# Optimization experiments

Measured on AMD Instinct MI355X. Metric: run time of the kernel, lower is better.

The kernel has to match this reference:

```python
import jax, jax.numpy as jnp
from jax import lax
import numpy as np

B, C, H, W, T = 8, 256, 31, 31, 7  # batch, channels, search HxW, template size


def setup_inputs() -> dict:
    key = jax.random.key(0)
    k1, k2, k3, k4 = jax.random.split(key, 4)
    sr = jax.random.normal(k1, (B, C, H, W), jnp.float32)
    tmpl = jax.random.normal(k2, (B, C, T, T), jnp.float32)
    # offset/mask conv params (module zero-inits; use small random as a trained stand-in)
    w_om = jax.random.normal(k3, (3 * T * T, C, 3, 3), jnp.float32) * 0.01
    b_om = jax.random.normal(k4, (3 * T * T,), jnp.float32) * 0.01
    return {"sr_features": sr, "template_features": tmpl,
            "w_offset_mask": w_om, "b_offset_mask": b_om}


def _modulated_deform_xcorr(sr, tmpl, w_om, b_om):
    Bs, Cs, Hs, Ws = sr.shape
    Ts = tmpl.shape[-1]
    K = Ts * Ts
    # 3x3 'same' conv predicting per-pixel offsets (y, x) and modulation mask
    om = lax.conv_general_dilated(sr, w_om, (1, 1), 'SAME',
                                  dimension_numbers=('NCHW', 'OIHW', 'NCHW'))
    om = om + b_om[None, :, None, None]
    off_y, off_x, mask = om[:, :K], om[:, K:2 * K], om[:, 2 * K:]
    mask = jax.nn.sigmoid(mask)
    oh, ow = Hs - Ts + 1, Ws - Ts + 1  # stride 1, padding 0, dilation 1
    off_y = off_y[:, :, :oh, :ow]
    off_x = off_x[:, :, :oh, :ow]
    mask = mask[:, :, :oh, :ow]
    # kernel-tap base offsets (k = p*T + q)
    ky = jnp.repeat(jnp.arange(Ts), Ts).astype(sr.dtype)  # (K,)
    kx = jnp.tile(jnp.arange(Ts), Ts).astype(sr.dtype)    # (K,)
    iy = jnp.arange(oh, dtype=sr.dtype)
    ix = jnp.arange(ow, dtype=sr.dtype)
    ys = iy[None, None, :, None] + ky[None, :, None, None] + off_y  # (B,K,oh,ow)
    xs = ix[None, None, None, :] + kx[None, :, None, None] + off_x  # (B,K,oh,ow)
    y0 = jnp.floor(ys)
    x0 = jnp.floor(xs)
    wy = ys - y0
    wx = xs - x0
    bidx = jnp.arange(Bs)[:, None, None, None]

    def gather(yf, xf):
        # zero-padded gather at integer corner (yf, xf); returns (B,K,oh,ow,C)
        valid = (yf >= 0) & (yf <= Hs - 1) & (xf >= 0) & (xf <= Ws - 1)
        yc = jnp.clip(yf, 0, Hs - 1).astype(jnp.int32)
        xc = jnp.clip(xf, 0, Ws - 1).astype(jnp.int32)
        v = sr[bidx, :, yc, xc]  # (B,K,oh,ow,C)
        return v * valid[..., None].astype(sr.dtype)

    one = jnp.asarray(1, sr.dtype)
    v = (((one - wy) * (one - wx))[..., None] * gather(y0, x0)
         + ((one - wy) * wx)[..., None] * gather(y0, x0 + 1)
         + (wy * (one - wx))[..., None] * gather(y0 + 1, x0)
         + (wy * wx)[..., None] * gather(y0 + 1, x0 + 1))
    # depthwise xcorr: template acts as per-(batch,channel) kernel, modulated by mask
    tmpl_k = tmpl.reshape(Bs, Cs, K)
    out = jnp.einsum('bck,bkij,bkijc->bcij', tmpl_k, mask, v)  # (B,C,oh,ow)
    return out


def reference(sr_features, template_features, w_offset_mask, b_offset_mask):
    return _modulated_deform_xcorr(sr_features, template_features,
                                   w_offset_mask, b_offset_mask)
```

## Files before the change

### kernel.cpp

```cpp
#include <hip/hip_runtime.h>
#include <hip/hip_bf16.h>
#include <math.h>

#define B_ 8
#define C_ 256
#define H_ 31
#define W_ 31
#define T_ 7
#define K_ 49
#define OC_ 147
#define OCP 160
#define OH_ 25
#define OW_ 25
#define NSP 961
#define OSP 625
#define KK_ 2304

typedef __bf16 bf16x8 __attribute__((ext_vector_type(8)));
typedef float f32x4 __attribute__((ext_vector_type(4)));

#define OFFB_SRT 0
#define OFFB_TMT 3936256
#define OFFB_WPK 4136960
#define OFFB_BIAS 4874240
#define OFFB_OM  4874880

__device__ inline float blo(unsigned u) { return __uint_as_float(u << 16); }
__device__ inline float bhi(unsigned u) { return __uint_as_float(u & 0xffff0000u); }

__global__ __launch_bounds__(256) void prep(const float* __restrict__ sr,
                                            const float* __restrict__ tm,
                                            const float* __restrict__ w,
                                            const float* __restrict__ bias,
                                            __hip_bfloat16* __restrict__ srT,
                                            __hip_bfloat16* __restrict__ tmT,
                                            __hip_bfloat16* __restrict__ wPk,
                                            float* __restrict__ biasP) {
    __shared__ float tile[32][33];
    int bid = blockIdx.x;
    int t = threadIdx.x;

    if (bid < 1984) {
        int b = bid / 248;
        int rem = bid % 248;
        int ct = rem / 31;
        int st = rem % 31;
        int c0 = ct * 32, s0 = st * 32;
        int tx = t & 31, ty = t >> 5;
        #pragma unroll
        for (int rr = 0; rr < 4; rr++) {
            int c = c0 + ty + rr * 8;
            int s = s0 + tx;
            if (s < NSP) tile[ty + rr * 8][tx] = sr[(b * C_ + c) * NSP + s];
        }
        __syncthreads();
        #pragma unroll
        for (int rr = 0; rr < 4; rr++) {
            int s = s0 + ty + rr * 8;
            int c = c0 + tx;
            if (s < NSP) srT[((long)b * NSP + s) * C_ + c] = __float2bfloat16(tile[tx][ty + rr * 8]);
        }
    } else if (bid < 2376) {
        int bx = bid - 1984;
        int b = bx / K_;
        int k = bx % K_;
        tmT[(b * K_ + k) * C_ + t] = __float2bfloat16(tm[(b * C_ + t) * K_ + k]);
    } else {
        if (bid == 2376 && t < OCP)
            biasP[t] = (t < OC_) ? bias[t] : 0.f;
        int i = (bid - 2376) * 256 + t;
        if (i < 46080) {
            int l = i & 63;
            int fid = i >> 6;
            int mf = fid % 5;
            int mh = (fid / 5) % 2;
            int ks = (fid / 10) % 2;
            int s  = (fid / 20) % 9;
            int cg = fid / 180;
            int oc = mh * 80 + mf * 16 + (l & 15);
            int cbase = cg * 64 + ks * 32 + (l >> 4) * 8;
            bf16x8 v;
            #pragma unroll
            for (int jj = 0; jj < 8; jj++) {
                float f = (oc < OC_) ? w[oc * KK_ + (cbase + jj) * 9 + s] : 0.f;
                v[jj] = (__bf16)f;
            }
            *reinterpret_cast<bf16x8*>(wPk + ((long)i << 3)) = v;
        }
    }
}

__global__ __launch_bounds__(128) void k3_mfma(const __hip_bfloat16* __restrict__ srT,
                                               const __hip_bfloat16* __restrict__ wPk,
                                               float* __restrict__ om) {
    __shared__ __hip_bfloat16 lds[88 * 72];
    int sb = (blockIdx.x & 7) * 100 + (blockIdx.x >> 3);
    int b = sb / 100;
    int rem = sb % 100;
    int i = rem / 4;
    int cg = rem % 4;
    int tid = threadIdx.x;

    const __hip_bfloat16* srTb = srT + (long)b * NSP * C_ + cg * 64;
    for (int o = tid; o < 648; o += 128) {
        int ryx = o >> 3;
        int c8 = (o & 7) * 8;
        int yy = ryx / 27;
        int xi = ryx - yy * 27;
        int y = i - 1 + yy;
        int x = xi - 1;
        bf16x8 v = {};
        if (y >= 0 && x >= 0)
            v = *reinterpret_cast<const bf16x8*>(srTb + (y * W_ + x) * C_ + c8);
        *reinterpret_cast<bf16x8*>(&lds[ryx * 72 + c8]) = v;
    }
    __syncthreads();

    int wv = tid >> 6;
    int l = tid & 63;
    int lr = l & 15, lg = l >> 4;

    f32x4 acc[5][2] = {};
    const bf16x8* apk = reinterpret_cast<const bf16x8*>(wPk);

    #pragma unroll
    for (int dy = 0; dy < 3; ++dy) {
        #pragma unroll
        for (int dx = 0; dx < 3; ++dx) {
            int s = dy * 3 + dx;
            #pragma unroll
            for (int ks = 0; ks < 2; ++ks) {
                int e0 = (dy * 27 + dx + lr) * 72 + ks * 32 + lg * 8;
                bf16x8 b0 = *reinterpret_cast<const bf16x8*>(&lds[e0]);
                bf16x8 b1 = *reinterpret_cast<const bf16x8*>(&lds[e0 + 16 * 72]);
                const bf16x8* ap = apk + (long)((((cg * 9 + s) * 2 + ks) * 2 + wv) * 5) * 64 + l;
                #pragma unroll
                for (int mf = 0; mf < 5; ++mf) {
                    bf16x8 a = ap[mf * 64];
                    acc[mf][0] = __builtin_amdgcn_mfma_f32_16x16x32_bf16(a, b0, acc[mf][0], 0, 0, 0);
                    acc[mf][1] = __builtin_amdgcn_mfma_f32_16x16x32_bf16(a, b1, acc[mf][1], 0, 0, 0);
                }
            }
        }
    }

    #pragma unroll
    for (int nf = 0; nf < 2; ++nf) {
        int j = nf * 16 + lr;
        if (j < OW_) {
            float* ob = om + (long)((b * OH_ + i) * 4 + cg) * (OW_ * OCP) + j * OCP + wv * 80 + lg * 4;
            #pragma unroll
            for (int mf = 0; mf < 5; ++mf)
                *reinterpret_cast<f32x4*>(ob + mf * 16) = acc[mf][nf];
        }
    }
}

__global__ __launch_bounds__(64) void k4_gather(const __hip_bfloat16* __restrict__ srT,
                                                const __hip_bfloat16* __restrict__ tmT,
                                                const float* __restrict__ om,
                                                const float* __restrict__ biasP,
                                                float* __restrict__ out) {
    __shared__ float lom[OCP];
    __shared__ int4 loff[K_];
    __shared__ float4 lwt[K_];
    int sb = (blockIdx.x & 7) * 625 + (blockIdx.x >> 3);
    int b = sb / OSP;
    int rem = sb % OSP;
    int i = rem / OW_;
    int j = rem % OW_;
    int t = threadIdx.x;

    if (t < 40) {
        f32x4 s = *reinterpret_cast<const f32x4*>(biasP + t * 4);
        const float* ob = om + (long)(b * OH_ + i) * (4 * OW_ * OCP) + j * OCP + t * 4;
        #pragma unroll
        for (int cg = 0; cg < 4; cg++)
            s += *reinterpret_cast<const f32x4*>(ob + cg * (OW_ * OCP));
        *reinterpret_cast<f32x4*>(lom + t * 4) = s;
    }
    __syncthreads();

    if (t < K_) {
        float oy = lom[t];
        float ox = lom[K_ + t];
        float mk = 1.f / (1.f + expf(-lom[2 * K_ + t]));
        float ys = (float)(i + t / T_) + oy;
        float xs = (float)(j + t % T_) + ox;
        float y0f = floorf(ys);
        float x0f = floorf(xs);
        float wy = ys - y0f, wx = xs - x0f;
        bool vy0 = (y0f >= 0.f) && (y0f <= 30.f);
        bool vy1 = (y0f >= -1.f) && (y0f <= 29.f);
        bool vx0 = (x0f >= 0.f) && (x0f <= 30.f);
        bool vx1 = (x0f >= -1.f) && (x0f <= 29.f);
        int iy = (int)y0f;
        int ix = (int)x0f;
        int cy0 = min(max(iy, 0), 30), cy1 = min(max(iy + 1, 0), 30);
        int cx0 = min(max(ix, 0), 30), cx1 = min(max(ix + 1, 0), 30);
        float a00 = (1.f - wy) * (1.f - wx), a01 = (1.f - wy) * wx;
        float a10 = wy * (1.f - wx), a11 = wy * wx;
        lwt[t] = make_float4(mk * a00 * (float)(vy0 && vx0),
                             mk * a01 * (float)(vy0 && vx1),
                             mk * a10 * (float)(vy1 && vx0),
                             mk * a11 * (float)(vy1 && vx1));
        loff[t] = make_int4((cy0 * W_ + cx0) * 64, (cy0 * W_ + cx1) * 64,
                            (cy1 * W_ + cx0) * 64, (cy1 * W_ + cx1) * 64);
    }
    __syncthreads();

    const uint2* srU = reinterpret_cast<const uint2*>(srT) + (long)b * NSP * 64;
    const uint2* tmU = reinterpret_cast<const uint2*>(tmT) + (long)b * K_ * 64;
    float a0 = 0.f, a1 = 0.f, a2 = 0.f, a3 = 0.f;

    for (int k = 0; k < K_; ++k) {
        int4 o = loff[k];
        float4 wt = lwt[k];
        uint2 u00 = srU[o.x + t];
        uint2 u01 = srU[o.y + t];
        uint2 u10 = srU[o.z + t];
        uint2 u11 = srU[o.w + t];
        uint2 tu  = tmU[(k << 6) + t];
        float s;
        s = wt.x * blo(u00.x); s = fmaf(wt.y, blo(u01.x), s);
        s = fmaf(wt.z, blo(u10.x), s); s = fmaf(wt.w, blo(u11.x), s);
        a0 = fmaf(blo(tu.x), s, a0);
        s = wt.x * bhi(u00.x); s = fmaf(wt.y, bhi(u01.x), s);
        s = fmaf(wt.z, bhi(u10.x), s); s = fmaf(wt.w, bhi(u11.x), s);
        a1 = fmaf(bhi(tu.x), s, a1);
        s = wt.x * blo(u00.y); s = fmaf(wt.y, blo(u01.y), s);
        s = fmaf(wt.z, blo(u10.y), s); s = fmaf(wt.w, blo(u11.y), s);
        a2 = fmaf(blo(tu.y), s, a2);
        s = wt.x * bhi(u00.y); s = fmaf(wt.y, bhi(u01.y), s);
        s = fmaf(wt.z, bhi(u10.y), s); s = fmaf(wt.w, bhi(u11.y), s);
        a3 = fmaf(bhi(tu.y), s, a3);
    }

    long ob = ((long)(b * C_ + 4 * t) * OH_ + i) * OW_ + j;
    out[ob] = a0;
    out[ob + OSP] = a1;
    out[ob + 2 * OSP] = a2;
    out[ob + 3 * OSP] = a3;
}

extern "C" void kernel_launch(void* const* d_in, const int* in_sizes, int n_in,
                              void* d_out, int out_size, void* d_ws, size_t ws_size,
                              hipStream_t stream) {
    const float* sr = (const float*)d_in[0];
    const float* tm = (const float*)d_in[1];
    const float* w  = (const float*)d_in[2];
    const float* bs = (const float*)d_in[3];
    float* out = (float*)d_out;
    char* wsb = (char*)d_ws;
    __hip_bfloat16* srT = (__hip_bfloat16*)(wsb + OFFB_SRT);
    __hip_bfloat16* tmT = (__hip_bfloat16*)(wsb + OFFB_TMT);
    __hip_bfloat16* wPk = (__hip_bfloat16*)(wsb + OFFB_WPK);
    float* biasP = (float*)(wsb + OFFB_BIAS);
    float* om = (float*)(wsb + OFFB_OM);

    prep<<<2556, 256, 0, stream>>>(sr, tm, w, bs, srT, tmT, wPk, biasP);
    k3_mfma<<<B_ * OH_ * 4, 128, 0, stream>>>(srT, wPk, om);
    k4_gather<<<B_ * OSP, 64, 0, stream>>>(srT, tmT, om, biasP, out);
}
```

Measured before the change: 139.6 us.

## Pack four pixels per block and split taps across half-waves with 16B loads

```diff
diff --git a/kernel.cpp b/kernel.cpp
--- a/kernel.cpp
+++ b/kernel.cpp
@@ -156,91 +156,118 @@
     }
 }
 
-__global__ __launch_bounds__(64) void k4_gather(const __hip_bfloat16* __restrict__ srT,
-                                                const __hip_bfloat16* __restrict__ tmT,
-                                                const float* __restrict__ om,
-                                                const float* __restrict__ biasP,
-                                                float* __restrict__ out) {
-    __shared__ float lom[OCP];
-    __shared__ int4 loff[K_];
-    __shared__ float4 lwt[K_];
-    int sb = (blockIdx.x & 7) * 625 + (blockIdx.x >> 3);
-    int b = sb / OSP;
-    int rem = sb % OSP;
-    int i = rem / OW_;
-    int j = rem % OW_;
-    int t = threadIdx.x;
-
-    if (t < 40) {
-        f32x4 s = *reinterpret_cast<const f32x4*>(biasP + t * 4);
-        const float* ob = om + (long)(b * OH_ + i) * (4 * OW_ * OCP) + j * OCP + t * 4;
+__global__ __launch_bounds__(256) void k4_gather(const __hip_bfloat16* __restrict__ srT,
+                                                 const __hip_bfloat16* __restrict__ tmT,
+                                                 const float* __restrict__ om,
+                                                 const float* __restrict__ biasP,
+                                                 float* __restrict__ out) {
+    __shared__ float lom[4][OCP];
+    __shared__ int4 loff[4][52];
+    __shared__ float4 lwt[4][52];
+    int wvp = threadIdx.x >> 6;
+    int l = threadIdx.x & 63;
+    int blk = (blockIdx.x & 7) * 157 + (blockIdx.x >> 3);
+    int pix = blk * 4 + wvp;
+    bool active = pix < B_ * OSP;
+    int b = 0, i = 0, j = 0;
+    if (active) {
+        b = pix / OSP;
+        int rem = pix % OSP;
+        i = rem / OW_;
+        j = rem % OW_;
+    }
+
+    if (active && l < 40) {
+        f32x4 s = *reinterpret_cast<const f32x4*>(biasP + l * 4);
+        const float* ob = om + (long)(b * OH_ + i) * (4 * OW_ * OCP) + j * OCP + l * 4;
         #pragma unroll
         for (int cg = 0; cg < 4; cg++)
             s += *reinterpret_cast<const f32x4*>(ob + cg * (OW_ * OCP));
-        *reinterpret_cast<f32x4*>(lom + t * 4) = s;
+        *reinterpret_cast<f32x4*>(&lom[wvp][l * 4]) = s;
     }
     __syncthreads();
 
-    if (t < K_) {
-        float oy = lom[t];
-        float ox = lom[K_ + t];
-        float mk = 1.f / (1.f + expf(-lom[2 * K_ + t]));
-        float ys = (float)(i + t / T_) + oy;
-        float xs = (float)(j + t % T_) + ox;
-        float y0f = floorf(ys);
-        float x0f = floorf(xs);
-        float wy = ys - y0f, wx = xs - x0f;
-        bool vy0 = (y0f >= 0.f) && (y0f <= 30.f);
-        bool vy1 = (y0f >= -1.f) && (y0f <= 29.f);
-        bool vx0 = (x0f >= 0.f) && (x0f <= 30.f);
-        bool vx1 = (x0f >= -1.f) && (x0f <= 29.f);
-        int iy = (int)y0f;
-        int ix = (int)x0f;
-        int cy0 = min(max(iy, 0), 30), cy1 = min(max(iy + 1, 0), 30);
-        int cx0 = min(max(ix, 0), 30), cx1 = min(max(ix + 1, 0), 30);
-        float a00 = (1.f - wy) * (1.f - wx), a01 = (1.f - wy) * wx;
-        float a10 = wy * (1.f - wx), a11 = wy * wx;
-        lwt[t] = make_float4(mk * a00 * (float)(vy0 && vx0),
-                             mk * a01 * (float)(vy0 && vx1),
-                             mk * a10 * (float)(vy1 && vx0),
-                             mk * a11 * (float)(vy1 && vx1));
-        loff[t] = make_int4((cy0 * W_ + cx0) * 64, (cy0 * W_ + cx1) * 64,
-                            (cy1 * W_ + cx0) * 64, (cy1 * W_ + cx1) * 64);
+    if (active && l < 50) {
+        if (l < K_) {
+            float oy = lom[wvp][l];
+            float ox = lom[wvp][K_ + l];
+            float mk = 1.f / (1.f + expf(-lom[wvp][2 * K_ + l]));
+            float ys = (float)(i + l / T_) + oy;
+            float xs = (float)(j + l % T_) + ox;
+            float y0f = floorf(ys);
+            float x0f = floorf(xs);
+            float wy = ys - y0f, wx = xs - x0f;
+            bool vy0 = (y0f >= 0.f) && (y0f <= 30.f);
+            bool vy1 = (y0f >= -1.f) && (y0f <= 29.f);
+            bool vx0 = (x0f >= 0.f) && (x0f <= 30.f);
+            bool vx1 = (x0f >= -1.f) && (x0f <= 29.f);
+            int iy = (int)y0f;
+            int ix = (int)x0f;
+            int cy0 = min(max(iy, 0), 30), cy1 = min(max(iy + 1, 0), 30);
+            int cx0 = min(max(ix, 0), 30), cx1 = min(max(ix + 1, 0), 30);
+            float a00 = (1.f - wy) * (1.f - wx), a01 = (1.f - wy) * wx;
+            float a10 = wy * (1.f - wx), a11 = wy * wx;
+            lwt[wvp][l] = make_float4(mk * a00 * (float)(vy0 && vx0),
+                                      mk * a01 * (float)(vy0 && vx1),
+                                      mk * a10 * (float)(vy1 && vx0),
+                                      mk * a11 * (float)(vy1 && vx1));
+            loff[wvp][l] = make_int4((cy0 * W_ + cx0) * 512, (cy0 * W_ + cx1) * 512,
+                                     (cy1 * W_ + cx0) * 512, (cy1 * W_ + cx1) * 512);
+        } else {
+            lwt[wvp][l] = make_float4(0.f, 0.f, 0.f, 0.f);
+            loff[wvp][l] = make_int4(0, 0, 0, 0);
+        }
     }
     __syncthreads();
-
-    const uint2* srU = reinterpret_cast<const uint2*>(srT) + (long)b * NSP * 64;
-    const uint2* tmU = reinterpret_cast<const uint2*>(tmT) + (long)b * K_ * 64;
-    float a0 = 0.f, a1 = 0.f, a2 = 0.f, a3 = 0.f;
-
-    for (int k = 0; k < K_; ++k) {
-        int4 o = loff[k];
-        float4 wt = lwt[k];
-        uint2 u00 = srU[o.x + t];
-        uint2 u01 = srU[o.y + t];
-        uint2 u10 = srU[o.z + t];
-        uint2 u11 = srU[o.w + t];
-        uint2 tu  = tmU[(k << 6) + t];
-        float s;
-        s = wt.x * blo(u00.x); s = fmaf(wt.y, blo(u01.x), s);
-        s = fmaf(wt.z, blo(u10.x), s); s = fmaf(wt.w, blo(u11.x), s);
-        a0 = fmaf(blo(tu.x), s, a0);
-        s = wt.x * bhi(u00.x); s = fmaf(wt.y, bhi(u01.x), s);
-        s = fmaf(wt.z, bhi(u10.x), s); s = fmaf(wt.w, bhi(u11.x), s);
-        a1 = fmaf(bhi(tu.x), s, a1);
-        s = wt.x * blo(u00.y); s = fmaf(wt.y, blo(u01.y), s);
-        s = fmaf(wt.z, blo(u10.y), s); s = fmaf(wt.w, blo(u11.y), s);
-        a2 = fmaf(blo(tu.y), s, a2);
-        s = wt.x * bhi(u00.y); s = fmaf(wt.y, bhi(u01.y), s);
-        s = fmaf(wt.z, bhi(u10.y), s); s = fmaf(wt.w, bhi(u11.y), s);
-        a3 = fmaf(bhi(tu.y), s, a3);
-    }
-
-    long ob = ((long)(b * C_ + 4 * t) * OH_ + i) * OW_ + j;
-    out[ob] = a0;
-    out[ob + OSP] = a1;
-    out[ob + 2 * OSP] = a2;
-    out[ob + 3 * OSP] = a3;
+    if (!active) return;
+
+    const char* srBase = (const char*)srT + (long)b * NSP * 512;
+    const char* tmBase = (const char*)tmT + (long)b * K_ * 512;
+    int half = l >> 5;
+    unsigned laneb = (unsigned)(l & 31) << 4;
+    float acc[8];
+    #pragma unroll
+    for (int q = 0; q < 8; q++) acc[q] = 0.f;
+
+    for (int k = 0; k < 50; k += 2) {
+        int keff = k + half;
+        int4 o = loff[wvp][keff];
+        float4 wt = lwt[wvp][keff];
+        uint4 u00 = *reinterpret_cast<const uint4*>(srBase + (unsigned)o.x + laneb);
+        uint4 u01 = *reinterpret_cast<const uint4*>(srBase + (unsigned)o.y + laneb);
+        uint4 u10 = *reinterpret_cast<const uint4*>(srBase + (unsigned)o.z + laneb);
+        uint4 u11 = *reinterpret_cast<const uint4*>(srBase + (unsigned)o.w + laneb);
+        uint4 tu  = *reinterpret_cast<const uint4*>(tmBase + ((unsigned)keff << 9) + laneb);
+        unsigned a_[4] = {u00.x, u00.y, u00.z, u00.w};
+        unsigned b_[4] = {u01.x, u01.y, u01.z, u01.w};
+        unsigned c_[4] = {u10.x, u10.y, u10.z, u10.w};
+        unsigned d_[4] = {u11.x, u11.y, u11.z, u11.w};
+        unsigned t_[4] = {tu.x, tu.y, tu.z, tu.w};
+        #pragma unroll
+        for (int q = 0; q < 4; q++) {
+            float s0 = wt.x * blo(a_[q]);
+            s0 = fmaf(wt.y, blo(b_[q]), s0);
+            s0 = fmaf(wt.z, blo(c_[q]), s0);
+            s0 = fmaf(wt.w, blo(d_[q]), s0);
+            acc[2 * q] = fmaf(blo(t_[q]), s0, acc[2 * q]);
+            float s1 = wt.x * bhi(a_[q]);
+            s1 = fmaf(wt.y, bhi(b_[q]), s1);
+            s1 = fmaf(wt.z, bhi(c_[q]), s1);
+            s1 = fmaf(wt.w, bhi(d_[q]), s1);
+            acc[2 * q + 1] = fmaf(bhi(t_[q]), s1, acc[2 * q + 1]);
+        }
+    }
+
+    #pragma unroll
+    for (int q = 0; q < 8; q++) acc[q] += __shfl_xor(acc[q], 32, 64);
+
+    if (l < 32) {
+        int c0 = l * 8;
+        long ob = ((long)(b * C_ + c0) * OH_ + i) * OW_ + j;
+        #pragma unroll
+        for (int q = 0; q < 8; q++)
+            out[ob + (long)q * OSP] = acc[q];
+    }
 }
 
 extern "C" void kernel_launch(void* const* d_in, const int* in_sizes, int n_in,
@@ -260,5 +287,5 @@
 
     prep<<<2556, 256, 0, stream>>>(sr, tm, w, bs, srT, tmT, wPk, biasP);
     k3_mfma<<<B_ * OH_ * 4, 128, 0, stream>>>(srT, wPk, om);
-    k4_gather<<<B_ * OSP, 64, 0, stream>>>(srT, tmT, om, biasP, out);
-}
+    k4_gather<<<1256, 256, 0, stream>>>(srT, tmT, om, biasP, out);
+}
```

Measured after the change: 122.9 us. 1.14x faster.
